# Kernel tuning notes

Measured on AMD Instinct MI355X. Metric: run time of the kernel, lower is better.

The kernel has to match this reference:

```python
import jax, jax.numpy as jnp
import numpy as np

DIM = 1024
NUM_EXPERTS = 8
TOP_K = 2
B, S = 2, 2048
HID = 4 * DIM


def setup_inputs() -> dict:
    key = jax.random.key(0)
    ks = jax.random.split(key, 7)
    scale = 0.02
    x = jax.random.normal(ks[0], (B, S, DIM), dtype=jnp.float32)
    gate_w = jax.random.normal(ks[1], (DIM, NUM_EXPERTS), dtype=jnp.float32) * scale
    gate_b = jnp.zeros((NUM_EXPERTS,), dtype=jnp.float32)
    w1 = jax.random.normal(ks[2], (NUM_EXPERTS, DIM, HID), dtype=jnp.float32) * scale
    b1 = jnp.zeros((NUM_EXPERTS, HID), dtype=jnp.float32)
    w2 = jax.random.normal(ks[3], (NUM_EXPERTS, HID, DIM), dtype=jnp.float32) * scale
    b2 = jnp.zeros((NUM_EXPERTS, DIM), dtype=jnp.float32)
    return {"x": x, "gate_w": gate_w, "gate_b": gate_b,
            "w1": w1, "b1": b1, "w2": w2, "b2": b2}


def reference(x, gate_w, gate_b, w1, b1, w2, b2):
    # Gate: [B,S,E]
    gates = jnp.einsum('bsd,de->bse', x, gate_w) + gate_b
    top_w, top_idx = jax.lax.top_k(gates, TOP_K)          # [B,S,K]
    probs = jax.nn.softmax(top_w, axis=-1)                # softmax over selected logits
    # Dense all-expert FFN (matches original: every expert runs on every token)
    h = jnp.einsum('bsd,edh->bseh', x, w1) + b1           # [B,S,E,4D]
    h = jax.nn.gelu(h, approximate=False)                 # exact GELU (torch default)
    y = jnp.einsum('bseh,ehd->bsed', h, w2) + b2          # [B,S,E,D]
    # Select top-k experts per token and combine
    sel = jnp.take_along_axis(y, top_idx[..., None], axis=2)   # [B,S,K,D]
    return jnp.sum(sel * probs[..., None], axis=2)        # [B,S,D]
```

## Files before the change

### kernel.cpp

```cpp
#include <hip/hip_runtime.h>
#include <hip/hip_bf16.h>

#define T_TOKENS 4096
#define DIM      1024
#define HID      4096
#define NE       8
#define CAP      4096
#define SPLITS   4
#define KSP      (HID / SPLITS)

typedef __attribute__((ext_vector_type(8))) short  bf16x8;
typedef __attribute__((ext_vector_type(4))) float  f32x4;
typedef __attribute__((ext_vector_type(4))) ushort u16x4;

__device__ static inline ushort f2bf(float f) {
    __hip_bfloat16 h = __float2bfloat16(f);
    return *(ushort*)&h;
}

__device__ static inline void gll16(const void* g, void* l) {
    __builtin_amdgcn_global_load_lds(
        (const __attribute__((address_space(1))) void*)g,
        (__attribute__((address_space(3))) void*)l,
        16, 0, 0);
}

#define MFMA16(a, b, c) __builtin_amdgcn_mfma_f32_16x16x32_bf16((a), (b), (c), 0, 0, 0)

__global__ __launch_bounds__(64) void gate_kernel(
    const float* __restrict__ x, const float* __restrict__ gw,
    const float* __restrict__ gb, __hip_bfloat16* __restrict__ xb,
    int* __restrict__ counts, int* __restrict__ tlist, float* __restrict__ plist)
{
    const int tok = blockIdx.x;
    const int l   = threadIdx.x;
    const float* xr = x + (size_t)tok * DIM;

    float part[NE];
#pragma unroll
    for (int e = 0; e < NE; e++) part[e] = 0.f;

#pragma unroll
    for (int i = 0; i < DIM / 64; i++) {
        int d = i * 64 + l;
        float xv = xr[d];
        xb[(size_t)tok * DIM + d] = __float2bfloat16(xv);
        const float4* g4 = (const float4*)(gw + (size_t)d * NE);
        float4 a = g4[0], b = g4[1];
        part[0] += xv * a.x; part[1] += xv * a.y;
        part[2] += xv * a.z; part[3] += xv * a.w;
        part[4] += xv * b.x; part[5] += xv * b.y;
        part[6] += xv * b.z; part[7] += xv * b.w;
    }
#pragma unroll
    for (int off = 32; off > 0; off >>= 1) {
#pragma unroll
        for (int e = 0; e < NE; e++) part[e] += __shfl_xor(part[e], off, 64);
    }
    if (l == 0) {
        float lg[NE];
#pragma unroll
        for (int e = 0; e < NE; e++) lg[e] = part[e] + gb[e];
        int i0 = 0;
#pragma unroll
        for (int e = 1; e < NE; e++) if (lg[e] > lg[i0]) i0 = e;
        int i1 = (i0 == 0) ? 1 : 0;
#pragma unroll
        for (int e = 0; e < NE; e++) if (e != i0 && lg[e] > lg[i1]) i1 = e;
        float t  = expf(lg[i1] - lg[i0]);
        float p0 = 1.f / (1.f + t);
        float p1 = t / (1.f + t);
        int pos0 = atomicAdd(&counts[i0], 1);
        tlist[i0 * CAP + pos0] = tok;              plist[i0 * CAP + pos0] = p0;
        int pos1 = atomicAdd(&counts[i1], 1);
        tlist[i1 * CAP + pos1] = tok | (1 << 15);  plist[i1 * CAP + pos1] = p1;
    }
}

__global__ void finalize_kernel(const int* __restrict__ counts, int* __restrict__ base)
{
    if (threadIdx.x == 0) {
        int acc = 0;
        for (int e = 0; e < NE; e++) { base[e] = acc; acc += counts[e]; }
        base[NE] = acc;
    }
}

__global__ __launch_bounds__(256) void transpose_cvt64(
    const float* __restrict__ in, __hip_bfloat16* __restrict__ outp, int K, int N)
{
    __shared__ ushort tile[64][68];
    const int e  = blockIdx.z;
    const float* src = in + (size_t)e * K * N;
    ushort* dst = (ushort*)outp + (size_t)e * K * N;
    const int k0 = blockIdx.y * 64, n0 = blockIdx.x * 64;
    const int tid = threadIdx.x;

    const int rn4 = (tid & 15) * 4;
    const int rk  = tid >> 4;
#pragma unroll
    for (int p = 0; p < 4; p++) {
        int k = rk + p * 16;
        float4 v = *(const float4*)&src[(size_t)(k0 + k) * N + n0 + rn4];
        tile[k][rn4 + 0] = f2bf(v.x);
        tile[k][rn4 + 1] = f2bf(v.y);
        tile[k][rn4 + 2] = f2bf(v.z);
        tile[k][rn4 + 3] = f2bf(v.w);
    }
    __syncthreads();
    const int wk4 = (tid & 15) * 4;
    const int wn  = tid >> 4;
#pragma unroll
    for (int p = 0; p < 4; p++) {
        int n = wn + p * 16;
        u16x4 u;
        u[0] = tile[wk4 + 0][n];
        u[1] = tile[wk4 + 1][n];
        u[2] = tile[wk4 + 2][n];
        u[3] = tile[wk4 + 3][n];
        *(u16x4*)&dst[(size_t)(n0 + n) * K + k0 + wk4] = u;
    }
}


#define AOFFc(d,s) (((d)*2+(s))*4096)
#define BOFFc(d,s) (16384 + ((d)*2+(s))*4096)

#define MFMA_CL(nj0, nj1)                                                    \
    _Pragma("unroll")                                                        \
    for (int mi = 0; mi < 4; mi++) {                                         \
        acc[mi][nj0] = MFMA16(af[mi], bf##nj0, acc[mi][nj0]);                \
        acc[mi][nj1] = MFMA16(af[mi], bf##nj1, acc[mi][nj1]);                \
    }

#define GEMM_CORE(NT, srcA0, srcA1, srcB0, srcB1)                            \
    f32x4 acc[4][4];                                                         \
    _Pragma("unroll")                                                        \
    for (int i = 0; i < 4; i++)                                              \
        _Pragma("unroll")                                                    \
        for (int j = 0; j < 4; j++) acc[i][j] = (f32x4){0.f,0.f,0.f,0.f};    \
    const int a0 = (wr * 64 + lm) * 32 + rch;                                \
    const int b0 = (wc * 64 + lm) * 32 + rch;                                \
    gll16(srcA0,      &lds[AOFFc(0,0) + w*1024]);                            \
    gll16(srcA1,      &lds[AOFFc(0,0) + w*1024 + 512]);                      \
    gll16(srcB0,      &lds[BOFFc(0,0) + w*1024]);                            \
    gll16(srcB1,      &lds[BOFFc(0,0) + w*1024 + 512]);                      \
    gll16(srcA0 + 32, &lds[AOFFc(0,1) + w*1024]);                            \
    gll16(srcA1 + 32, &lds[AOFFc(0,1) + w*1024 + 512]);                      \
    gll16(srcB0 + 32, &lds[BOFFc(0,1) + w*1024]);                            \
    gll16(srcB1 + 32, &lds[BOFFc(0,1) + w*1024 + 512]);                      \
    asm volatile("s_waitcnt vmcnt(4)" ::: "memory");                         \
    gll16(srcA0 + 64, &lds[AOFFc(1,0) + w*1024]);                            \
    gll16(srcA1 + 64, &lds[AOFFc(1,0) + w*1024 + 512]);                      \
    gll16(srcB0 + 64, &lds[BOFFc(1,0) + w*1024]);                            \
    gll16(srcB1 + 64, &lds[BOFFc(1,0) + w*1024 + 512]);                      \
    gll16(srcA0 + 96, &lds[AOFFc(1,1) + w*1024]);                            \
    gll16(srcA1 + 96, &lds[AOFFc(1,1) + w*1024 + 512]);                      \
    asm volatile("s_waitcnt vmcnt(6)" ::: "memory");                         \
    __builtin_amdgcn_s_barrier();                                            \
    _Pragma("unroll 1")                                                      \
    for (int t = 0; t < NT; t++) {                                           \
        const int d   = t & 1;                                               \
        const int aof  = d * 8192,        bof  = 16384 + d * 8192;           \
        const int bofN = 16384 + (d^1) * 8192;                               \
        bf16x8 af[4]; bf16x8 bf0, bf1, bf2, bf3;                             \
                          \
        _Pragma("unroll")                                                    \
        for (int mi = 0; mi < 4; mi++)                                       \
            af[mi] = *(const bf16x8*)&lds[aof + a0 + mi*512];                \
        bf0 = *(const bf16x8*)&lds[bof + b0];                                \
        bf1 = *(const bf16x8*)&lds[bof + b0 + 512];                          \
        if (t + 1 < NT) {                                                    \
            size_t ko = (size_t)(t+1)*64 + 32;                               \
            gll16(srcB0 + ko, &lds[bofN + 4096 + w*1024]);                   \
            gll16(srcB1 + ko, &lds[bofN + 4096 + w*1024 + 512]);             \
        }                                                                    \
        __builtin_amdgcn_s_barrier();                                        \
        __builtin_amdgcn_s_setprio(1);                                       \
        MFMA_CL(0, 1)                                                        \
        __builtin_amdgcn_s_setprio(0);                                       \
        __builtin_amdgcn_s_barrier();                                        \
                                    \
        bf2 = *(const bf16x8*)&lds[bof + b0 + 1024];                         \
        bf3 = *(const bf16x8*)&lds[bof + b0 + 1536];                         \
        if (t + 2 < NT) {                                                    \
            size_t ko = (size_t)(t+2)*64;                                    \
            gll16(srcA0 + ko, &lds[aof + w*1024]);                           \
            gll16(srcA1 + ko, &lds[aof + w*1024 + 512]);                     \
        }                                                                    \
        __builtin_amdgcn_s_barrier();                                        \
        __builtin_amdgcn_s_setprio(1);                                       \
        MFMA_CL(2, 3)                                                        \
        __builtin_amdgcn_s_setprio(0);                                       \
        __builtin_amdgcn_s_barrier();                                        \
                          \
        _Pragma("unroll")                                                    \
        for (int mi = 0; mi < 4; mi++)                                       \
            af[mi] = *(const bf16x8*)&lds[aof + 4096 + a0 + mi*512];         \
        bf0 = *(const bf16x8*)&lds[bof + 4096 + b0];                         \
        bf1 = *(const bf16x8*)&lds[bof + 4096 + b0 + 512];                   \
        if (t + 2 < NT) {                                                    \
            size_t ko = (size_t)(t+2)*64;                                    \
            gll16(srcB0 + ko, &lds[bof + w*1024]);                           \
            gll16(srcB1 + ko, &lds[bof + w*1024 + 512]);                     \
        }                                                                    \
        __builtin_amdgcn_s_barrier();                                        \
        __builtin_amdgcn_s_setprio(1);                                       \
        MFMA_CL(0, 1)                                                        \
        __builtin_amdgcn_s_setprio(0);                                       \
        __builtin_amdgcn_s_barrier();                                        \
                      \
        bf2 = *(const bf16x8*)&lds[bof + 4096 + b0 + 1024];                  \
        bf3 = *(const bf16x8*)&lds[bof + 4096 + b0 + 1536];                  \
        if (t + 2 < NT) {                                                    \
            size_t ko = (size_t)(t+2)*64 + 32;                               \
            gll16(srcA0 + ko, &lds[aof + 4096 + w*1024]);                    \
            gll16(srcA1 + ko, &lds[aof + 4096 + w*1024 + 512]);              \
        }                                                                    \
        __builtin_amdgcn_s_barrier();                                        \
        __builtin_amdgcn_s_setprio(1);                                       \
        MFMA_CL(2, 3)                                                        \
        __builtin_amdgcn_s_setprio(0);                                       \
        if (t < NT - 2) { asm volatile("s_waitcnt vmcnt(6)" ::: "memory"); } \
        else            { asm volatile("s_waitcnt vmcnt(0)" ::: "memory"); } \
        __builtin_amdgcn_s_barrier();                                        \
    }

#define CORE_IDX                                                             \
    const int tid = threadIdx.x;                                             \
    const int l = tid & 63, w = tid >> 6;                                    \
    const int wr = w >> 1, wc = w & 1;                                       \
    const int lm = l & 15, kg = l >> 4;                                      \
    const int rch = (kg ^ ((lm >> 1) & 3)) * 8;                              \
    const int p0c  = w * 128 + l;                                            \
    const int srow = p0c >> 2;                 \
    const int sch  = p0c & 3;                                                \
    const int sc0  = (sch ^ ((srow >> 1) & 3)) * 8;

__global__ __launch_bounds__(256, 2) void ffn1_kernel(
    const __hip_bfloat16* __restrict__ xb, const __hip_bfloat16* __restrict__ w1t,
    const float* __restrict__ b1, const int* __restrict__ counts,
    const int* __restrict__ base, const int* __restrict__ tlist,
    int* __restrict__ tickets, __hip_bfloat16* __restrict__ H)
{
    __shared__ __align__(16) ushort lds[32768];
    __shared__ int s_task;
    CORE_IDX
    const int e  = blockIdx.x & 7;
    const int ne = counts[e];
    const int mt = (ne + 127) >> 7;
    const int ntask = mt * 32;
    const int hb = base[e];
    if (mt == 0) return;

    for (;;) {
        __syncthreads();
        if (tid == 0) s_task = atomicAdd(&tickets[e], 1);
        __syncthreads();
        const int i = s_task;
        if (i >= ntask) break;
        const int cb = i / mt, rb = i - cb * mt;

        const int r0g = rb * 128 + srow;
        const int r1g = r0g + 16;
        const int tok0 = tlist[e * CAP + (r0g < ne ? r0g : ne - 1)] & 0xFFF;
        const int tok1 = tlist[e * CAP + (r1g < ne ? r1g : ne - 1)] & 0xFFF;
        const ushort* srcA0 = (const ushort*)xb + (size_t)tok0 * DIM + sc0;
        const ushort* srcA1 = (const ushort*)xb + (size_t)tok1 * DIM + sc0;
        const ushort* srcB0 = (const ushort*)w1t + ((size_t)e * HID + cb * 128 + srow) * DIM + sc0;
        const ushort* srcB1 = srcB0 + (size_t)16 * DIM;

        GEMM_CORE(16, srcA0, srcA1, srcB0, srcB1)

#pragma unroll
        for (int nj = 0; nj < 4; nj++) {
            int col = wc * 64 + nj * 16 + lm;
            float bias = b1[e * HID + cb * 128 + col];
#pragma unroll
            for (int mi = 0; mi < 4; mi++) {
#pragma unroll
                for (int jj = 0; jj < 4; jj++) {
                    int row = wr * 64 + mi * 16 + kg * 4 + jj;
                    float vv = acc[mi][nj][jj] + bias;
                    vv = 0.5f * vv * (1.0f + erff(vv * 0.70710678118654752f));
                    lds[row * 128 + (col ^ ((row & 12) << 2))] = f2bf(vv);
                }
            }
        }
        __syncthreads();
#pragma unroll
        for (int pch = 0; pch < 8; pch++) {
            int c   = pch * 256 + tid;
            int row = c >> 4, seg = c & 15;
            int r   = rb * 128 + row;
            if (r < ne) {
                int pseg = seg ^ ((row & 12) >> 1);
                bf16x8 vv8 = *(const bf16x8*)&lds[row * 128 + pseg * 8];
                *(bf16x8*)((ushort*)H + (size_t)(hb + r) * HID + cb * 128 + seg * 8) = vv8;
            }
        }
    }
}

__global__ __launch_bounds__(256, 2) void ffn2_kernel(
    const __hip_bfloat16* __restrict__ H, const __hip_bfloat16* __restrict__ w2t,
    const float* __restrict__ b2, const int* __restrict__ counts,
    const int* __restrict__ base, const int* __restrict__ tlist,
    const float* __restrict__ plist, int* __restrict__ tickets,
    __hip_bfloat16* __restrict__ Y)
{
    __shared__ __align__(16) ushort lds[32768];
    __shared__ int s_task;
    CORE_IDX
    const int e  = blockIdx.x & 7;
    const int ne = counts[e];
    const int mt = (ne + 127) >> 7;
    const int ntask = mt * 32;
    const int hb = base[e];
    if (mt == 0) return;

    for (;;) {
        __syncthreads();
        if (tid == 0) s_task = atomicAdd(&tickets[NE + e], 1);
        __syncthreads();
        const int i = s_task;
        if (i >= ntask) break;
        const int c  = i / mt, rb = i - c * mt;
        const int sp = c >> 3, cb = c & 7;

        const int r0g = rb * 128 + srow;
        const int r1g = r0g + 16;
        const int hr0 = hb + (r0g < ne ? r0g : ne - 1);
        const int hr1 = hb + (r1g < ne ? r1g : ne - 1);
        const size_t ko0 = (size_t)sp * KSP;
        const ushort* srcA0 = (const ushort*)H + (size_t)hr0 * HID + ko0 + sc0;
        const ushort* srcA1 = (const ushort*)H + (size_t)hr1 * HID + ko0 + sc0;
        const ushort* srcB0 = (const ushort*)w2t + ((size_t)e * DIM + cb * 128 + srow) * HID + ko0 + sc0;
        const ushort* srcB1 = srcB0 + (size_t)16 * HID;

        GEMM_CORE(16, srcA0, srcA1, srcB0, srcB1)

#pragma unroll
        for (int nj = 0; nj < 4; nj++) {
            int col = wc * 64 + nj * 16 + lm;
            float bias = (sp == 0) ? b2[e * DIM + cb * 128 + col] : 0.f;
#pragma unroll
            for (int mi = 0; mi < 4; mi++) {
#pragma unroll
                for (int jj = 0; jj < 4; jj++) {
                    int row = wr * 64 + mi * 16 + kg * 4 + jj;
                    int r   = rb * 128 + row;
                    float p = plist[e * CAP + (r < ne ? r : ne - 1)];
                    float vv = (acc[mi][nj][jj] + bias) * p;
                    lds[row * 128 + (col ^ ((row & 12) << 2))] = f2bf(vv);
                }
            }
        }
        __syncthreads();
#pragma unroll
        for (int pch = 0; pch < 8; pch++) {
            int cch = pch * 256 + tid;
            int row = cch >> 4, seg = cch & 15;
            int r   = rb * 128 + row;
            if (r < ne) {
                int tv  = tlist[e * CAP + r];
                int tok = tv & 0xFFF, kk = tv >> 15;
                int pseg = seg ^ ((row & 12) >> 1);
                bf16x8 vv8 = *(const bf16x8*)&lds[row * 128 + pseg * 8];
                *(bf16x8*)((ushort*)Y + ((size_t)(kk * 4 + sp) * T_TOKENS + tok) * DIM
                           + cb * 128 + seg * 8) = vv8;
            }
        }
    }
}

__global__ __launch_bounds__(256) void reduce_kernel(
    const __hip_bfloat16* __restrict__ Y, float* __restrict__ out)
{
    const size_t i = ((size_t)blockIdx.x * 256 + threadIdx.x) * 8;
    float s[8];
#pragma unroll
    for (int j = 0; j < 8; j++) s[j] = 0.f;
#pragma unroll
    for (int sl = 0; sl < 8; sl++) {
        bf16x8 v = *(const bf16x8*)((const ushort*)Y + (size_t)sl * T_TOKENS * DIM + i);
#pragma unroll
        for (int j = 0; j < 8; j++) {
            union { unsigned int ui; float f; } cv;
            cv.ui = ((unsigned int)(ushort)v[j]) << 16;
            s[j] += cv.f;
        }
    }
#pragma unroll
    for (int j = 0; j < 8; j++) out[i + j] = s[j];
}

extern "C" void kernel_launch(void* const* d_in, const int* in_sizes, int n_in,
                              void* d_out, int out_size, void* d_ws, size_t ws_size,
                              hipStream_t stream)
{
    const float* x  = (const float*)d_in[0];
    const float* gw = (const float*)d_in[1];
    const float* gb = (const float*)d_in[2];
    const float* w1 = (const float*)d_in[3];
    const float* b1 = (const float*)d_in[4];
    const float* w2 = (const float*)d_in[5];
    const float* b2 = (const float*)d_in[6];
    float* out = (float*)d_out;

    char* ws = (char*)d_ws;
    __hip_bfloat16* w1t = (__hip_bfloat16*)(ws);
    __hip_bfloat16* w2t = (__hip_bfloat16*)(ws + 67108864);
    __hip_bfloat16* Hb  = (__hip_bfloat16*)(ws + 134217728);
    __hip_bfloat16* xb  = (__hip_bfloat16*)(ws + 201326592);
    int*   tlist  = (int*)  (ws + 209715200);
    float* plist  = (float*)(ws + 209846272);
    int*   counts = (int*)  (ws + 209977344);
    int*   basep  = (int*)  (ws + 209977408);
    int*   tickets= (int*)  (ws + 209977472);
    __hip_bfloat16* Y = (__hip_bfloat16*)(ws);

    hipMemsetAsync(counts, 0, 192, stream);

    gate_kernel<<<T_TOKENS, 64, 0, stream>>>(x, gw, gb, xb, counts, tlist, plist);
    finalize_kernel<<<1, 64, 0, stream>>>(counts, basep);

    transpose_cvt64<<<dim3(HID / 64, DIM / 64, NE), 256, 0, stream>>>(w1, w1t, DIM, HID);
    transpose_cvt64<<<dim3(DIM / 64, HID / 64, NE), 256, 0, stream>>>(w2, w2t, HID, DIM);

    ffn1_kernel<<<512, 256, 0, stream>>>(
        xb, w1t, b1, counts, basep, tlist, tickets, Hb);
    ffn2_kernel<<<512, 256, 0, stream>>>(
        Hb, w2t, b2, counts, basep, tlist, plist, tickets, Y);
    reduce_kernel<<<(T_TOKENS * DIM / 8) / 256, 256, 0, stream>>>(Y, out);
}
```

Before: 469.5 us.

## Replace hand-scheduled GEMM pipeline with simple double buffer and raise occupancy

Swaps the hand-scheduled multi-stage GEMM main loop in both FFN kernels for a plain double-buffered loop. The old loop had two 32-wide k sub-tiles per iteration, split MFMA clusters, priority toggles and explicit vmcnt waits; the new one stages one 32-wide k slice per buffer. This halves shared memory per block, so launch bounds go to three blocks per CU and both persistent grids grow to 768 blocks. The aim is more latency hiding through occupancy instead of manual scheduling. In exchange it adds a full __syncthreads per k step and no longer overlaps loads with MFMA clusters as finely.

```diff
diff --git a/kernel.cpp b/kernel.cpp
--- a/kernel.cpp
+++ b/kernel.cpp
@@ -123,107 +123,47 @@
 }
 
 
-#define AOFFc(d,s) (((d)*2+(s))*4096)
-#define BOFFc(d,s) (16384 + ((d)*2+(s))*4096)
-
-#define MFMA_CL(nj0, nj1)                                                    \
+#define MFMA_ALL                                                             \
     _Pragma("unroll")                                                        \
-    for (int mi = 0; mi < 4; mi++) {                                         \
-        acc[mi][nj0] = MFMA16(af[mi], bf##nj0, acc[mi][nj0]);                \
-        acc[mi][nj1] = MFMA16(af[mi], bf##nj1, acc[mi][nj1]);                \
-    }
-
-#define GEMM_CORE(NT, srcA0, srcA1, srcB0, srcB1)                            \
+    for (int mi = 0; mi < 4; mi++)                                           \
+        _Pragma("unroll")                                                    \
+        for (int nj = 0; nj < 4; nj++)                                       \
+            acc[mi][nj] = MFMA16(af[mi], bfr[nj], acc[mi][nj]);
+
+#define GEMM_CORE(NK, srcA0, srcA1, srcB0, srcB1)                            \
     f32x4 acc[4][4];                                                         \
     _Pragma("unroll")                                                        \
     for (int i = 0; i < 4; i++)                                              \
         _Pragma("unroll")                                                    \
         for (int j = 0; j < 4; j++) acc[i][j] = (f32x4){0.f,0.f,0.f,0.f};    \
-    const int a0 = (wr * 64 + lm) * 32 + rch;                                \
-    const int b0 = (wc * 64 + lm) * 32 + rch;                                \
-    gll16(srcA0,      &lds[AOFFc(0,0) + w*1024]);                            \
-    gll16(srcA1,      &lds[AOFFc(0,0) + w*1024 + 512]);                      \
-    gll16(srcB0,      &lds[BOFFc(0,0) + w*1024]);                            \
-    gll16(srcB1,      &lds[BOFFc(0,0) + w*1024 + 512]);                      \
-    gll16(srcA0 + 32, &lds[AOFFc(0,1) + w*1024]);                            \
-    gll16(srcA1 + 32, &lds[AOFFc(0,1) + w*1024 + 512]);                      \
-    gll16(srcB0 + 32, &lds[BOFFc(0,1) + w*1024]);                            \
-    gll16(srcB1 + 32, &lds[BOFFc(0,1) + w*1024 + 512]);                      \
-    asm volatile("s_waitcnt vmcnt(4)" ::: "memory");                         \
-    gll16(srcA0 + 64, &lds[AOFFc(1,0) + w*1024]);                            \
-    gll16(srcA1 + 64, &lds[AOFFc(1,0) + w*1024 + 512]);                      \
-    gll16(srcB0 + 64, &lds[BOFFc(1,0) + w*1024]);                            \
-    gll16(srcB1 + 64, &lds[BOFFc(1,0) + w*1024 + 512]);                      \
-    gll16(srcA0 + 96, &lds[AOFFc(1,1) + w*1024]);                            \
-    gll16(srcA1 + 96, &lds[AOFFc(1,1) + w*1024 + 512]);                      \
-    asm volatile("s_waitcnt vmcnt(6)" ::: "memory");                         \
-    __builtin_amdgcn_s_barrier();                                            \
+    gll16(srcA0, &lds[lo0]);        gll16(srcA1, &lds[lo1]);                 \
+    gll16(srcB0, &lds[8192 + lo0]); gll16(srcB1, &lds[8192 + lo1]);          \
+    int cur = 0;                                                             \
     _Pragma("unroll 1")                                                      \
-    for (int t = 0; t < NT; t++) {                                           \
-        const int d   = t & 1;                                               \
-        const int aof  = d * 8192,        bof  = 16384 + d * 8192;           \
-        const int bofN = 16384 + (d^1) * 8192;                               \
-        bf16x8 af[4]; bf16x8 bf0, bf1, bf2, bf3;                             \
-                          \
+    for (int ks = 0; ks < NK; ks++) {                                        \
+        __syncthreads();                                                     \
+        if (ks + 1 < NK) {                                                   \
+            const int ko = (ks + 1) * 32;                                    \
+            const int nb = (cur ^ 1) * 4096;                                 \
+            gll16(srcA0 + ko, &lds[nb + lo0]);                               \
+            gll16(srcA1 + ko, &lds[nb + lo1]);                               \
+            gll16(srcB0 + ko, &lds[8192 + nb + lo0]);                        \
+            gll16(srcB1 + ko, &lds[8192 + nb + lo1]);                        \
+        }                                                                    \
+        const int cb_ = cur * 4096;                                          \
+        bf16x8 af[4], bfr[4];                                                \
         _Pragma("unroll")                                                    \
-        for (int mi = 0; mi < 4; mi++)                                       \
-            af[mi] = *(const bf16x8*)&lds[aof + a0 + mi*512];                \
-        bf0 = *(const bf16x8*)&lds[bof + b0];                                \
-        bf1 = *(const bf16x8*)&lds[bof + b0 + 512];                          \
-        if (t + 1 < NT) {                                                    \
-            size_t ko = (size_t)(t+1)*64 + 32;                               \
-            gll16(srcB0 + ko, &lds[bofN + 4096 + w*1024]);                   \
-            gll16(srcB1 + ko, &lds[bofN + 4096 + w*1024 + 512]);             \
+        for (int mi = 0; mi < 4; mi++) {                                     \
+            int row = wr * 64 + mi * 16 + lm;                                \
+            af[mi] = *(const bf16x8*)&lds[cb_ + row * 32 + rch];             \
         }                                                                    \
-        __builtin_amdgcn_s_barrier();                                        \
-        __builtin_amdgcn_s_setprio(1);                                       \
-        MFMA_CL(0, 1)                                                        \
-        __builtin_amdgcn_s_setprio(0);                                       \
-        __builtin_amdgcn_s_barrier();                                        \
-                                    \
-        bf2 = *(const bf16x8*)&lds[bof + b0 + 1024];                         \
-        bf3 = *(const bf16x8*)&lds[bof + b0 + 1536];                         \
-        if (t + 2 < NT) {                                                    \
-            size_t ko = (size_t)(t+2)*64;                                    \
-            gll16(srcA0 + ko, &lds[aof + w*1024]);                           \
-            gll16(srcA1 + ko, &lds[aof + w*1024 + 512]);                     \
+        _Pragma("unroll")                                                    \
+        for (int nj = 0; nj < 4; nj++) {                                     \
+            int row = wc * 64 + nj * 16 + lm;                                \
+            bfr[nj] = *(const bf16x8*)&lds[8192 + cb_ + row * 32 + rch];     \
         }                                                                    \
-        __builtin_amdgcn_s_barrier();                                        \
-        __builtin_amdgcn_s_setprio(1);                                       \
-        MFMA_CL(2, 3)                                                        \
-        __builtin_amdgcn_s_setprio(0);                                       \
-        __builtin_amdgcn_s_barrier();                                        \
-                          \
-        _Pragma("unroll")                                                    \
-        for (int mi = 0; mi < 4; mi++)                                       \
-            af[mi] = *(const bf16x8*)&lds[aof + 4096 + a0 + mi*512];         \
-        bf0 = *(const bf16x8*)&lds[bof + 4096 + b0];                         \
-        bf1 = *(const bf16x8*)&lds[bof + 4096 + b0 + 512];                   \
-        if (t + 2 < NT) {                                                    \
-            size_t ko = (size_t)(t+2)*64;                                    \
-            gll16(srcB0 + ko, &lds[bof + w*1024]);                           \
-            gll16(srcB1 + ko, &lds[bof + w*1024 + 512]);                     \
-        }                                                                    \
-        __builtin_amdgcn_s_barrier();                                        \
-        __builtin_amdgcn_s_setprio(1);                                       \
-        MFMA_CL(0, 1)                                                        \
-        __builtin_amdgcn_s_setprio(0);                                       \
-        __builtin_amdgcn_s_barrier();                                        \
-                      \
-        bf2 = *(const bf16x8*)&lds[bof + 4096 + b0 + 1024];                  \
-        bf3 = *(const bf16x8*)&lds[bof + 4096 + b0 + 1536];                  \
-        if (t + 2 < NT) {                                                    \
-            size_t ko = (size_t)(t+2)*64 + 32;                               \
-            gll16(srcA0 + ko, &lds[aof + 4096 + w*1024]);                    \
-            gll16(srcA1 + ko, &lds[aof + 4096 + w*1024 + 512]);              \
-        }                                                                    \
-        __builtin_amdgcn_s_barrier();                                        \
-        __builtin_amdgcn_s_setprio(1);                                       \
-        MFMA_CL(2, 3)                                                        \
-        __builtin_amdgcn_s_setprio(0);                                       \
-        if (t < NT - 2) { asm volatile("s_waitcnt vmcnt(6)" ::: "memory"); } \
-        else            { asm volatile("s_waitcnt vmcnt(0)" ::: "memory"); } \
-        __builtin_amdgcn_s_barrier();                                        \
+        MFMA_ALL                                                             \
+        cur ^= 1;                                                            \
     }
 
 #define CORE_IDX                                                             \
@@ -232,18 +172,21 @@
     const int wr = w >> 1, wc = w & 1;                                       \
     const int lm = l & 15, kg = l >> 4;                                      \
     const int rch = (kg ^ ((lm >> 1) & 3)) * 8;                              \
-    const int p0c  = w * 128 + l;                                            \
-    const int srow = p0c >> 2;                 \
-    const int sch  = p0c & 3;                                                \
-    const int sc0  = (sch ^ ((srow >> 1) & 3)) * 8;
-
-__global__ __launch_bounds__(256, 2) void ffn1_kernel(
+    const int slot0 = w * 128 + l;                                           \
+    const int slot1 = w * 128 + 64 + l;                                      \
+    const int row0 = slot0 >> 2, row1 = slot1 >> 2;                          \
+    const int ch0 = ((slot0 & 3) ^ ((row0 >> 1) & 3)) * 8;                   \
+    const int ch1 = ((slot1 & 3) ^ ((row1 >> 1) & 3)) * 8;                   \
+    const int lo0 = w * 1024;                                                \
+    const int lo1 = w * 1024 + 512;
+
+__global__ __launch_bounds__(256, 3) void ffn1_kernel(
     const __hip_bfloat16* __restrict__ xb, const __hip_bfloat16* __restrict__ w1t,
     const float* __restrict__ b1, const int* __restrict__ counts,
     const int* __restrict__ base, const int* __restrict__ tlist,
     int* __restrict__ tickets, __hip_bfloat16* __restrict__ H)
 {
-    __shared__ __align__(16) ushort lds[32768];
+    __shared__ __align__(16) ushort lds[16384];
     __shared__ int s_task;
     CORE_IDX
     const int e  = blockIdx.x & 7;
@@ -261,17 +204,18 @@
         if (i >= ntask) break;
         const int cb = i / mt, rb = i - cb * mt;
 
-        const int r0g = rb * 128 + srow;
-        const int r1g = r0g + 16;
+        const int r0g = rb * 128 + row0;
+        const int r1g = rb * 128 + row1;
         const int tok0 = tlist[e * CAP + (r0g < ne ? r0g : ne - 1)] & 0xFFF;
         const int tok1 = tlist[e * CAP + (r1g < ne ? r1g : ne - 1)] & 0xFFF;
-        const ushort* srcA0 = (const ushort*)xb + (size_t)tok0 * DIM + sc0;
-        const ushort* srcA1 = (const ushort*)xb + (size_t)tok1 * DIM + sc0;
-        const ushort* srcB0 = (const ushort*)w1t + ((size_t)e * HID + cb * 128 + srow) * DIM + sc0;
-        const ushort* srcB1 = srcB0 + (size_t)16 * DIM;
-
-        GEMM_CORE(16, srcA0, srcA1, srcB0, srcB1)
-
+        const ushort* srcA0 = (const ushort*)xb + (size_t)tok0 * DIM + ch0;
+        const ushort* srcA1 = (const ushort*)xb + (size_t)tok1 * DIM + ch1;
+        const ushort* srcB0 = (const ushort*)w1t + ((size_t)e * HID + cb * 128 + row0) * DIM + ch0;
+        const ushort* srcB1 = (const ushort*)w1t + ((size_t)e * HID + cb * 128 + row1) * DIM + ch1;
+
+        GEMM_CORE(32, srcA0, srcA1, srcB0, srcB1)
+
+        __syncthreads();
 #pragma unroll
         for (int nj = 0; nj < 4; nj++) {
             int col = wc * 64 + nj * 16 + lm;
@@ -302,14 +246,14 @@
     }
 }
 
-__global__ __launch_bounds__(256, 2) void ffn2_kernel(
+__global__ __launch_bounds__(256, 3) void ffn2_kernel(
     const __hip_bfloat16* __restrict__ H, const __hip_bfloat16* __restrict__ w2t,
     const float* __restrict__ b2, const int* __restrict__ counts,
     const int* __restrict__ base, const int* __restrict__ tlist,
     const float* __restrict__ plist, int* __restrict__ tickets,
     __hip_bfloat16* __restrict__ Y)
 {
-    __shared__ __align__(16) ushort lds[32768];
+    __shared__ __align__(16) ushort lds[16384];
     __shared__ int s_task;
     CORE_IDX
     const int e  = blockIdx.x & 7;
@@ -328,18 +272,19 @@
         const int c  = i / mt, rb = i - c * mt;
         const int sp = c >> 3, cb = c & 7;
 
-        const int r0g = rb * 128 + srow;
-        const int r1g = r0g + 16;
+        const int r0g = rb * 128 + row0;
+        const int r1g = rb * 128 + row1;
         const int hr0 = hb + (r0g < ne ? r0g : ne - 1);
         const int hr1 = hb + (r1g < ne ? r1g : ne - 1);
         const size_t ko0 = (size_t)sp * KSP;
-        const ushort* srcA0 = (const ushort*)H + (size_t)hr0 * HID + ko0 + sc0;
-        const ushort* srcA1 = (const ushort*)H + (size_t)hr1 * HID + ko0 + sc0;
-        const ushort* srcB0 = (const ushort*)w2t + ((size_t)e * DIM + cb * 128 + srow) * HID + ko0 + sc0;
-        const ushort* srcB1 = srcB0 + (size_t)16 * HID;
-
-        GEMM_CORE(16, srcA0, srcA1, srcB0, srcB1)
-
+        const ushort* srcA0 = (const ushort*)H + (size_t)hr0 * HID + ko0 + ch0;
+        const ushort* srcA1 = (const ushort*)H + (size_t)hr1 * HID + ko0 + ch1;
+        const ushort* srcB0 = (const ushort*)w2t + ((size_t)e * DIM + cb * 128 + row0) * HID + ko0 + ch0;
+        const ushort* srcB1 = (const ushort*)w2t + ((size_t)e * DIM + cb * 128 + row1) * HID + ko0 + ch1;
+
+        GEMM_CORE(32, srcA0, srcA1, srcB0, srcB1)
+
+        __syncthreads();
 #pragma unroll
         for (int nj = 0; nj < 4; nj++) {
             int col = wc * 64 + nj * 16 + lm;
@@ -428,9 +373,9 @@
     transpose_cvt64<<<dim3(HID / 64, DIM / 64, NE), 256, 0, stream>>>(w1, w1t, DIM, HID);
     transpose_cvt64<<<dim3(DIM / 64, HID / 64, NE), 256, 0, stream>>>(w2, w2t, HID, DIM);
 
-    ffn1_kernel<<<512, 256, 0, stream>>>(
+    ffn1_kernel<<<768, 256, 0, stream>>>(
         xb, w1t, b1, counts, basep, tlist, tickets, Hb);
-    ffn2_kernel<<<512, 256, 0, stream>>>(
+    ffn2_kernel<<<768, 256, 0, stream>>>(
         Hb, w2t, b2, counts, basep, tlist, plist, tickets, Y);
     reduce_kernel<<<(T_TOKENS * DIM / 8) / 256, 256, 0, stream>>>(Y, out);
 }
```

Result: faster. 435.6 us (-7.2%).
